# Kernel optimization log

Measured on AMD Instinct MI355X. Metric: run time of the kernel, lower is better.

Reference implementation:

```python
import jax, jax.numpy as jnp
import numpy as np

B, T, HORIZON = 64, 12, 12
N, E, K, H = 1024, 8, 3, 64
DIN, DOUT, YCOV = 1, 1, 1


def setup_inputs() -> dict:
    key = jax.random.key(0)
    ks = jax.random.split(key, 8)

    def xavier(k, shape):
        std = (2.0 / (shape[0] + shape[1])) ** 0.5
        return jax.random.normal(k, shape, jnp.float32) * std

    return {
        "x": jax.random.normal(ks[0], (B, T, N, DIN), jnp.float32),
        "y_cov": jax.random.normal(ks[1], (B, HORIZON, N, YCOV), jnp.float32),
        "node_embeddings": jax.random.normal(ks[2], (N, E), jnp.float32),
        "enc_gate_W": xavier(ks[3], (K * (DIN + H), 2 * H)),
        "enc_gate_b": jnp.zeros((2 * H,), jnp.float32),
        "enc_upd_W": xavier(ks[4], (K * (DIN + H), H)),
        "enc_upd_b": jnp.zeros((H,), jnp.float32),
        "dec_gate_W": xavier(ks[5], (K * (DOUT + YCOV + H), 2 * H)),
        "dec_gate_b": jnp.zeros((2 * H,), jnp.float32),
        "dec_upd_W": xavier(ks[6], (K * (DOUT + YCOV + H), H)),
        "dec_upd_b": jnp.zeros((H,), jnp.float32),
        "proj_W": xavier(ks[7], (H, DOUT)),
        "proj_b": jnp.zeros((DOUT,), jnp.float32),
    }


def _cheb(support, k):
    # Chebyshev polynomial set: T0=I, T1=A, Tk = 2*A@T_{k-1} - T_{k-2}
    mats = [jnp.eye(support.shape[0], dtype=support.dtype), support]
    for _ in range(2, k):
        mats.append(2.0 * (support @ mats[-1]) - mats[-2])
    return jnp.stack(mats)  # [K, N, N]


def _gcn(x, supports, W, b):
    # x: [B,N,C]; supports: [K,N,N] -> gather [B,N,K,C], concat k-major as in torch.cat
    xg = jnp.einsum('knm,bmc->bnkc', supports, x)
    Bb, Nn, Kk, Cc = xg.shape
    return xg.reshape(Bb, Nn, Kk * Cc) @ W + b


def _cell(x, state, supports, gW, gb, uW, ub):
    zr = jax.nn.sigmoid(_gcn(jnp.concatenate([x, state], axis=-1), supports, gW, gb))
    z, r = jnp.split(zr, 2, axis=-1)
    hc = jnp.tanh(_gcn(jnp.concatenate([x, z * state], axis=-1), supports, uW, ub))
    return r * state + (1.0 - r) * hc


def reference(x, y_cov, node_embeddings, enc_gate_W, enc_gate_b, enc_upd_W,
              enc_upd_b, dec_gate_W, dec_gate_b, dec_upd_W, dec_upd_b,
              proj_W, proj_b):
    # adaptive adjacency: softmax(relu(E E^T), axis=1)
    support = jax.nn.softmax(jax.nn.relu(node_embeddings @ node_embeddings.T), axis=1)
    supports = _cheb(support, K)

    # encoder over T_in steps (single rnn layer)
    h0 = jnp.zeros((x.shape[0], N, H), x.dtype)

    def enc_step(h, xt):
        h = _cell(xt, h, supports, enc_gate_W, enc_gate_b, enc_upd_W, enc_upd_b)
        return h, None

    h_t, _ = jax.lax.scan(enc_step, h0, jnp.swapaxes(x, 0, 1))

    go0 = jnp.zeros((x.shape[0], N, DOUT), x.dtype)

    def dec_step(carry, yt):
        go, h = carry
        h = _cell(jnp.concatenate([go, yt], axis=-1), h, supports,
                  dec_gate_W, dec_gate_b, dec_upd_W, dec_upd_b)
        go = h @ proj_W + proj_b
        return (go, h), go

    _, outs = jax.lax.scan(dec_step, (go0, h_t), jnp.swapaxes(y_cov, 0, 1))
    return jnp.swapaxes(outs, 0, 1)  # [B, horizon, N, output_dim]
```

## Files before the change

kernel.cpp:

```cpp
#include <hip/hip_runtime.h>


typedef __attribute__((ext_vector_type(8))) short bf16x8;
typedef __attribute__((ext_vector_type(4))) float f32x4;
typedef __attribute__((ext_vector_type(4))) unsigned short u16x4;

__device__ __forceinline__ float b2f(unsigned short u) {
    union { unsigned int i; float f; } v; v.i = ((unsigned int)u) << 16; return v.f;
}
__device__ __forceinline__ unsigned short f2b(float f) {
    union { float f; unsigned int i; } v; v.f = f;
    unsigned int r = v.i + 0x7FFFu + ((v.i >> 16) & 1u);
    return (unsigned short)(r >> 16);
}

#define GLOAD_LDS16(g, l) __builtin_amdgcn_global_load_lds( \
    (const __attribute__((address_space(1))) void*)(g),     \
    (__attribute__((address_space(3))) void*)(l), 16, 0, 0)

__global__ __launch_bounds__(256) void gemm_bt(
    const unsigned short* __restrict__ P, int lda,
    const unsigned short* __restrict__ QT, int ldb,
    unsigned short* __restrict__ C, int ldc,
    int K, float scale)
{
    __shared__ __align__(16) unsigned short As[128 * 32];
    __shared__ __align__(16) unsigned short Bs[128 * 32];
    const int tid = threadIdx.x;
    const int m0 = blockIdx.y << 7, n0 = blockIdx.x << 7;
    const int w = tid >> 6, l = tid & 63;
    const int wm = (w >> 1) << 6, wn = (w & 1) << 6;
    const int lr = l & 15, lq = l >> 4;
    const int arow = tid >> 2, ak = (tid & 3) << 3;
    f32x4 acc[4][4] = {};

    for (int k0 = 0; k0 < K; k0 += 32) {
#pragma unroll
        for (int p = 0; p < 2; ++p)
            GLOAD_LDS16(P + (size_t)(m0 + arow + (p << 6)) * lda + k0 + ak,
                        &As[((arow + (p << 6)) << 5) + ak]);
#pragma unroll
        for (int p = 0; p < 2; ++p)
            GLOAD_LDS16(QT + (size_t)(n0 + arow + (p << 6)) * ldb + k0 + ak,
                        &Bs[((arow + (p << 6)) << 5) + ak]);
        __syncthreads();
        bf16x8 a[4], b[4];
#pragma unroll
        for (int i = 0; i < 4; ++i)
            a[i] = *(const bf16x8*)&As[((wm + (i << 4) + lr) << 5) + (lq << 3)];
#pragma unroll
        for (int j = 0; j < 4; ++j)
            b[j] = *(const bf16x8*)&Bs[((wn + (j << 4) + lr) << 5) + (lq << 3)];
#pragma unroll
        for (int i = 0; i < 4; ++i)
#pragma unroll
            for (int j = 0; j < 4; ++j)
                acc[i][j] = __builtin_amdgcn_mfma_f32_16x16x32_bf16(a[i], b[j], acc[i][j], 0, 0, 0);
        __syncthreads();
    }
#pragma unroll
    for (int i = 0; i < 4; ++i)
#pragma unroll
        for (int j = 0; j < 4; ++j)
#pragma unroll
            for (int r = 0; r < 4; ++r) {
                const int m = m0 + wm + (i << 4) + (lq << 2) + r;
                const int n = n0 + wn + (j << 4) + lr;
                C[(size_t)m * ldc + n] = f2b(acc[i][j][r] * scale);
            }
}

__global__ __launch_bounds__(256) void cell_gate(
    const unsigned short* __restrict__ AA, const unsigned short* __restrict__ XhT,
    const unsigned short* __restrict__ Hb, const unsigned short* __restrict__ WT,
    const float* __restrict__ bias, const float* __restrict__ wx,
    const float* __restrict__ xin, int t,
    const unsigned short* __restrict__ XSgT, int xsrow,
    const unsigned short* __restrict__ Go, const float* __restrict__ H32,
    const float* __restrict__ prW, const float* __restrict__ prb,
    float* __restrict__ Sgo,
    unsigned short* __restrict__ Zb, unsigned short* __restrict__ ZhT,
    float* __restrict__ R, int dec, int goflag)
{
    __shared__ __align__(16) unsigned short As[256 * 32];
    __shared__ __align__(16) unsigned short Bs[128 * 32];
    __shared__ __align__(16) unsigned short Shs[256 * 72];
    __shared__ float SgoS[256];
    const int tid = threadIdx.x;
    const int b = blockIdx.x >> 3, n0 = (blockIdx.x & 7) << 7;
    const int w = tid >> 6, l = tid & 63;
    const int lr = l & 15, lq = l >> 4;
    const int arow = tid >> 2, ak = (tid & 3) << 3;

    {
        const int wm = w << 6;
        f32x4 acc[4][4] = {};
        for (int k0 = 0; k0 < 1024; k0 += 32) {
#pragma unroll
            for (int p = 0; p < 4; ++p) {
                const int row = arow + (p << 6);
                const int grow = (p < 2) ? (n0 + row) : (896 + n0 + row);
                GLOAD_LDS16(AA + (size_t)grow * 1024 + k0 + ak, &As[(row << 5) + ak]);
            }
            GLOAD_LDS16(XhT + (size_t)((b << 6) + arow) * 1024 + k0 + ak,
                        &Bs[(arow << 5) + ak]);
            __syncthreads();
            bf16x8 a[4], bb[4];
#pragma unroll
            for (int i = 0; i < 4; ++i)
                a[i] = *(const bf16x8*)&As[((wm + (i << 4) + lr) << 5) + (lq << 3)];
#pragma unroll
            for (int j = 0; j < 4; ++j)
                bb[j] = *(const bf16x8*)&Bs[(((j << 4) + lr) << 5) + (lq << 3)];
#pragma unroll
            for (int i = 0; i < 4; ++i)
#pragma unroll
                for (int j = 0; j < 4; ++j)
                    acc[i][j] = __builtin_amdgcn_mfma_f32_16x16x32_bf16(a[i], bb[j], acc[i][j], 0, 0, 0);
            __syncthreads();
        }
#pragma unroll
        for (int i = 0; i < 4; ++i)
#pragma unroll
            for (int j = 0; j < 4; ++j)
#pragma unroll
                for (int r = 0; r < 4; ++r) {
                    const int m = wm + (i << 4) + (lq << 2) + r;
                    const int c = (j << 4) + lr;
                    Shs[m * 72 + c] = f2b(acc[i][j][r]);
                }
        if (dec) {
            float pw[4];
#pragma unroll
            for (int j = 0; j < 4; ++j) pw[j] = prW[(j << 4) + lr];
            const float pb0 = prb[0];
#pragma unroll
            for (int i = 0; i < 4; ++i)
#pragma unroll
                for (int r = 0; r < 4; ++r) {
                    float v = acc[i][0][r] * pw[0] + acc[i][1][r] * pw[1]
                            + acc[i][2][r] * pw[2] + acc[i][3][r] * pw[3];
                    v += __shfl_down(v, 8, 16);
                    v += __shfl_down(v, 4, 16);
                    v += __shfl_down(v, 2, 16);
                    v += __shfl_down(v, 1, 16);
                    if (lr == 0) {
                        const int m = wm + (i << 4) + (lq << 2) + r;
                        const int grow = (m < 128) ? (n0 + m) : (896 + n0 + m);
                        const float val = goflag
                            ? (v + pb0 * ((m < 128) ? 1.f : 2.f)) : 0.f;
                        Sgo[(size_t)grow * 64 + b] = val;
                        SgoS[m] = val;
                    }
                }
        }
    }

    const int wm2 = (w >> 1) << 6, wn2 = (w & 1) << 6;
    f32x4 acc2[4][4] = {};
    for (int kk0 = 0; kk0 < 192; kk0 += 32) {
#pragma unroll
        for (int p = 0; p < 2; ++p)
            GLOAD_LDS16(WT + (size_t)(arow + (p << 6)) * 192 + kk0 + ak,
                        &Bs[((arow + (p << 6)) << 5) + ak]);
        if (kk0 < 64) {
#pragma unroll
            for (int p = 0; p < 2; ++p)
                GLOAD_LDS16(Hb + ((size_t)(b << 10) + n0 + arow + (p << 6)) * 64 + kk0 + ak,
                            &As[((arow + (p << 6)) << 5) + ak]);
        }
        __syncthreads();
        bf16x8 a[4], bb[4];
        if (kk0 < 64) {
#pragma unroll
            for (int i = 0; i < 4; ++i)
                a[i] = *(const bf16x8*)&As[((wm2 + (i << 4) + lr) << 5) + (lq << 3)];
        } else {
            const int rowb = (kk0 >= 128) ? 128 : 0;
            const int c0 = kk0 & 63;
#pragma unroll
            for (int i = 0; i < 4; ++i)
                a[i] = *(const bf16x8*)&Shs[(rowb + wm2 + (i << 4) + lr) * 72 + c0 + (lq << 3)];
        }
#pragma unroll
        for (int j = 0; j < 4; ++j)
            bb[j] = *(const bf16x8*)&Bs[((wn2 + (j << 4) + lr) << 5) + (lq << 3)];
#pragma unroll
        for (int i = 0; i < 4; ++i)
#pragma unroll
            for (int j = 0; j < 4; ++j)
                acc2[i][j] = __builtin_amdgcn_mfma_f32_16x16x32_bf16(a[i], bb[j], acc2[i][j], 0, 0, 0);
        __syncthreads();
    }

#pragma unroll
    for (int i = 0; i < 4; ++i) {
        const int nb_loc = wm2 + (i << 4) + (lq << 2);
        const int node_base = n0 + nb_loc;
        float c0[4], c1[4], c2[4], c3[4], c4[4], c5[4];
        for (int r = 0; r < 4; ++r) {
            const int node = node_base + r;
            if (!dec) {
                c0[r] = xin[((b * 12 + t) << 10) + node];
                c1[r] = b2f(XSgT[(size_t)(xsrow + t * 64 + b) * 2048 + node]);
                c2[r] = b2f(XSgT[(size_t)(xsrow + t * 64 + b) * 2048 + 1024 + node]);
                c3[r] = c4[r] = c5[r] = 0.f;
            } else {
                c0[r] = b2f(Go[(b << 10) + node]);
                c1[r] = xin[((b * 12 + t) << 10) + node];
                c2[r] = SgoS[nb_loc + r];
                c3[r] = b2f(XSgT[(size_t)(xsrow + t * 64 + b) * 2048 + node]);
                c4[r] = SgoS[128 + nb_loc + r];
                c5[r] = b2f(XSgT[(size_t)(xsrow + t * 64 + b) * 2048 + 1024 + node]);
            }
        }
#pragma unroll
        for (int j = 0; j < 4; ++j) {
            const int jc = wn2 + (j << 4) + lr;
            const float bj = bias[jc];
            const float w0 = wx[jc], w1 = wx[128 + jc], w2 = wx[256 + jc];
            float w3 = 0.f, w4 = 0.f, w5 = 0.f;
            if (dec) { w3 = wx[384 + jc]; w4 = wx[512 + jc]; w5 = wx[640 + jc]; }
            if (jc < 64) {
                u16x4 pack;
                for (int r = 0; r < 4; ++r) {
                    float v = acc2[i][j][r] + bj + c0[r] * w0 + c1[r] * w1 + c2[r] * w2
                              + c3[r] * w3 + c4[r] * w4 + c5[r] * w5;
                    float g = 1.f / (1.f + __expf(-v));
                    const int node = node_base + r;
                    const size_t idx = ((size_t)(b << 10) + node) * 64 + jc;
                    float zh = g * H32[idx];
                    unsigned short zb = f2b(zh);
                    Zb[idx] = zb;
                    pack[r] = zb;
                }
                *(u16x4*)&ZhT[(size_t)((b << 6) + jc) * 1024 + node_base] = pack;
            } else {
                for (int r = 0; r < 4; ++r) {
                    float v = acc2[i][j][r] + bj + c0[r] * w0 + c1[r] * w1 + c2[r] * w2
                              + c3[r] * w3 + c4[r] * w4 + c5[r] * w5;
                    float g = 1.f / (1.f + __expf(-v));
                    const int node = node_base + r;
                    R[((size_t)(b << 10) + node) * 64 + (jc - 64)] = g;
                }
            }
        }
    }
}

__global__ __launch_bounds__(256) void cell_update(
    const unsigned short* __restrict__ AA, const unsigned short* __restrict__ ZhT,
    const unsigned short* __restrict__ Zb, const unsigned short* __restrict__ WT,
    const float* __restrict__ bias, const float* __restrict__ wx,
    const float* __restrict__ xin, int t,
    const unsigned short* __restrict__ XSgT, int xsrow,
    const float* __restrict__ Sgo, const float* __restrict__ Rg,
    float* __restrict__ H32, unsigned short* __restrict__ Hb,
    unsigned short* __restrict__ XhT,
    const float* __restrict__ prW, const float* __restrict__ prb,
    unsigned short* __restrict__ Go, float* __restrict__ outp, int dec)
{
    __shared__ __align__(16) unsigned short As[256 * 32];
    __shared__ __align__(16) unsigned short Bs[64 * 32];
    __shared__ __align__(16) unsigned short Shs[256 * 72];
    const int tid = threadIdx.x;
    const int b = blockIdx.x >> 3, n0 = (blockIdx.x & 7) << 7;
    const int w = tid >> 6, l = tid & 63;
    const int lr = l & 15, lq = l >> 4;
    const int arow = tid >> 2, ak = (tid & 3) << 3;

    {
        const int wm = w << 6;
        f32x4 acc[4][4] = {};
        for (int k0 = 0; k0 < 1024; k0 += 32) {
#pragma unroll
            for (int p = 0; p < 4; ++p) {
                const int row = arow + (p << 6);
                const int grow = (p < 2) ? (n0 + row) : (896 + n0 + row);
                GLOAD_LDS16(AA + (size_t)grow * 1024 + k0 + ak, &As[(row << 5) + ak]);
            }
            GLOAD_LDS16(ZhT + (size_t)((b << 6) + arow) * 1024 + k0 + ak,
                        &Bs[(arow << 5) + ak]);
            __syncthreads();
            bf16x8 a[4], bb[4];
#pragma unroll
            for (int i = 0; i < 4; ++i)
                a[i] = *(const bf16x8*)&As[((wm + (i << 4) + lr) << 5) + (lq << 3)];
#pragma unroll
            for (int j = 0; j < 4; ++j)
                bb[j] = *(const bf16x8*)&Bs[(((j << 4) + lr) << 5) + (lq << 3)];
#pragma unroll
            for (int i = 0; i < 4; ++i)
#pragma unroll
                for (int j = 0; j < 4; ++j)
                    acc[i][j] = __builtin_amdgcn_mfma_f32_16x16x32_bf16(a[i], bb[j], acc[i][j], 0, 0, 0);
            __syncthreads();
        }
#pragma unroll
        for (int i = 0; i < 4; ++i)
#pragma unroll
            for (int j = 0; j < 4; ++j)
#pragma unroll
                for (int r = 0; r < 4; ++r) {
                    const int m = wm + (i << 4) + (lq << 2) + r;
                    const int c = (j << 4) + lr;
                    Shs[m * 72 + c] = f2b(acc[i][j][r]);
                }
    }

    const int wm2 = w << 5;
    f32x4 acc2[2][4] = {};
    for (int kk0 = 0; kk0 < 192; kk0 += 32) {
        GLOAD_LDS16(WT + (size_t)arow * 192 + kk0 + ak, &Bs[(arow << 5) + ak]);
        if (kk0 < 64) {
#pragma unroll
            for (int p = 0; p < 2; ++p)
                GLOAD_LDS16(Zb + ((size_t)(b << 10) + n0 + arow + (p << 6)) * 64 + kk0 + ak,
                            &As[((arow + (p << 6)) << 5) + ak]);
        }
        __syncthreads();
        bf16x8 a[2], bb[4];
        if (kk0 < 64) {
#pragma unroll
            for (int i = 0; i < 2; ++i)
                a[i] = *(const bf16x8*)&As[((wm2 + (i << 4) + lr) << 5) + (lq << 3)];
        } else {
            const int rowb = (kk0 >= 128) ? 128 : 0;
            const int c0 = kk0 & 63;
#pragma unroll
            for (int i = 0; i < 2; ++i)
                a[i] = *(const bf16x8*)&Shs[(rowb + wm2 + (i << 4) + lr) * 72 + c0 + (lq << 3)];
        }
#pragma unroll
        for (int j = 0; j < 4; ++j)
            bb[j] = *(const bf16x8*)&Bs[(((j << 4) + lr) << 5) + (lq << 3)];
#pragma unroll
        for (int i = 0; i < 2; ++i)
#pragma unroll
            for (int j = 0; j < 4; ++j)
                acc2[i][j] = __builtin_amdgcn_mfma_f32_16x16x32_bf16(a[i], bb[j], acc2[i][j], 0, 0, 0);
        __syncthreads();
    }

    float pw[4];
    if (dec) {
#pragma unroll
        for (int j = 0; j < 4; ++j) pw[j] = prW[(j << 4) + lr];
    }

#pragma unroll
    for (int i = 0; i < 2; ++i) {
        const int node_base = n0 + wm2 + (i << 4) + (lq << 2);
        float c0[4], c1[4], c2[4], c3[4], c4[4], c5[4];
        for (int r = 0; r < 4; ++r) {
            const int node = node_base + r;
            if (!dec) {
                c0[r] = xin[((b * 12 + t) << 10) + node];
                c1[r] = b2f(XSgT[(size_t)(xsrow + t * 64 + b) * 2048 + node]);
                c2[r] = b2f(XSgT[(size_t)(xsrow + t * 64 + b) * 2048 + 1024 + node]);
                c3[r] = c4[r] = c5[r] = 0.f;
            } else {
                c0[r] = b2f(Go[(b << 10) + node]);
                c1[r] = xin[((b * 12 + t) << 10) + node];
                c2[r] = Sgo[(size_t)node * 64 + b];
                c3[r] = b2f(XSgT[(size_t)(xsrow + t * 64 + b) * 2048 + node]);
                c4[r] = Sgo[(size_t)(1024 + node) * 64 + b];
                c5[r] = b2f(XSgT[(size_t)(xsrow + t * 64 + b) * 2048 + 1024 + node]);
            }
        }
        float psum[4] = {0.f, 0.f, 0.f, 0.f};
#pragma unroll
        for (int j = 0; j < 4; ++j) {
            const int jc = (j << 4) + lr;
            const float bj = bias[jc];
            const float w0 = wx[jc], w1 = wx[64 + jc], w2 = wx[128 + jc];
            float w3 = 0.f, w4 = 0.f, w5 = 0.f;
            if (dec) { w3 = wx[192 + jc]; w4 = wx[256 + jc]; w5 = wx[320 + jc]; }
            u16x4 pack;
            for (int r = 0; r < 4; ++r) {
                float v = acc2[i][j][r] + bj + c0[r] * w0 + c1[r] * w1 + c2[r] * w2
                          + c3[r] * w3 + c4[r] * w4 + c5[r] * w5;
                float hc = tanhf(v);
                const int node = node_base + r;
                const size_t idx = ((size_t)(b << 10) + node) * 64 + jc;
                float rr = Rg[idx];
                float hn = rr * H32[idx] + (1.f - rr) * hc;
                H32[idx] = hn;
                unsigned short hb = f2b(hn);
                Hb[idx] = hb;
                pack[r] = hb;
                if (dec) psum[r] += hn * pw[j];
            }
            *(u16x4*)&XhT[(size_t)((b << 6) + jc) * 1024 + node_base] = pack;
        }
        if (dec) {
#pragma unroll
            for (int r = 0; r < 4; ++r) {
                float v = psum[r];
                v += __shfl_down(v, 8, 16);
                v += __shfl_down(v, 4, 16);
                v += __shfl_down(v, 2, 16);
                v += __shfl_down(v, 1, 16);
                if (lr == 0) {
                    const int node = node_base + r;
                    const float go = v + prb[0];
                    Go[(b << 10) + node] = f2b(go);
                    outp[((size_t)(b * 12 + t) << 10) + node] = go;
                }
            }
        }
    }
}

__global__ __launch_bounds__(256) void adj_softmax(
    const float* __restrict__ E, unsigned short* __restrict__ A)
{
    __shared__ float Es[8192];
    __shared__ float vals[1024];
    __shared__ float red[8];
    const int tid = threadIdx.x;
    const int r = blockIdx.x;
    for (int i = tid; i < 8192; i += 256) Es[i] = E[i];
    __syncthreads();
    float er[8];
#pragma unroll
    for (int e = 0; e < 8; ++e) er[e] = Es[(r << 3) + e];
    float lmax = -1e30f;
    for (int c = tid; c < 1024; c += 256) {
        float s = 0.f;
#pragma unroll
        for (int e = 0; e < 8; ++e) s += er[e] * Es[(c << 3) + e];
        s = fmaxf(s, 0.f);
        vals[c] = s;
        lmax = fmaxf(lmax, s);
    }
    for (int off = 32; off; off >>= 1) lmax = fmaxf(lmax, __shfl_down(lmax, off, 64));
    if ((tid & 63) == 0) red[tid >> 6] = lmax;
    __syncthreads();
    const float m = fmaxf(fmaxf(red[0], red[1]), fmaxf(red[2], red[3]));
    float lsum = 0.f;
    for (int c = tid; c < 1024; c += 256) {
        float e = __expf(vals[c] - m);
        vals[c] = e;
        lsum += e;
    }
    for (int off = 32; off; off >>= 1) lsum += __shfl_down(lsum, off, 64);
    if ((tid & 63) == 0) red[4 + (tid >> 6)] = lsum;
    __syncthreads();
    const float inv = 1.f / (red[4] + red[5] + red[6] + red[7]);
    for (int c = tid; c < 1024; c += 256)
        A[(r << 10) + c] = f2b(vals[c] * inv);
}

__global__ __launch_bounds__(256) void transpose_bf16(
    const unsigned short* __restrict__ src, unsigned short* __restrict__ dst)
{
    __shared__ unsigned short tile[64][65];
    const int bx = blockIdx.x & 15, by = blockIdx.x >> 4;
    const int x0 = bx << 6, y0 = by << 6;
    for (int i = threadIdx.x; i < 4096; i += 256) {
        const int r = i >> 6, c = i & 63;
        tile[r][c] = src[((y0 + r) << 10) + x0 + c];
    }
    __syncthreads();
    for (int i = threadIdx.x; i < 4096; i += 256) {
        const int r = i >> 6, c = i & 63;
        dst[((x0 + r) << 10) + y0 + c] = tile[c][r];
    }
}

__global__ __launch_bounds__(256) void build_xall(
    const float* __restrict__ x, const float* __restrict__ y,
    unsigned short* __restrict__ XallT)
{
    const int id = blockIdx.x * 256 + threadIdx.x;
    const int row = id >> 10, n = id & 1023;
    int t, b;
    const float* src;
    if (row < 768) { t = row >> 6; b = row & 63; src = x; }
    else { const int rr = row - 768; t = rr >> 6; b = rr & 63; src = y; }
    XallT[id] = f2b(src[((b * 12 + t) << 10) + n]);
}

__global__ __launch_bounds__(256) void wprep(
    const float* egW, const float* egb,
    const float* euW, const float* eub,
    const float* dgW, const float* dgb,
    const float* duW, const float* dub,
    const float* pW, const float* pb,
    unsigned short* WgTe, unsigned short* WuTe, unsigned short* WgTd, unsigned short* WuTd,
    float* wxge, float* wxue, float* wxgd, float* wxud,
    float* bge, float* bue, float* bgd, float* bud,
    float* projW, float* projb)
{
    const int tid0 = blockIdx.x * 256 + threadIdx.x;
    const int stride = 256 * gridDim.x;
    for (int i = tid0; i < 128 * 192; i += stride) {
        const int j = i / 192, kk = i % 192, k = kk >> 6, c = kk & 63;
        float v = egW[(k * 65 + 1 + c) * 128 + j];
        if (k == 0) v -= egW[(131 + c) * 128 + j];
        WgTe[i] = f2b(v);
    }
    for (int i = tid0; i < 64 * 192; i += stride) {
        const int j = i / 192, kk = i % 192, k = kk >> 6, c = kk & 63;
        float v = euW[(k * 65 + 1 + c) * 64 + j];
        if (k == 0) v -= euW[(131 + c) * 64 + j];
        WuTe[i] = f2b(v);
    }
    for (int i = tid0; i < 128 * 192; i += stride) {
        const int j = i / 192, kk = i % 192, k = kk >> 6, c = kk & 63;
        float v = dgW[(k * 66 + 2 + c) * 128 + j];
        if (k == 0) v -= dgW[(134 + c) * 128 + j];
        WgTd[i] = f2b(v);
    }
    for (int i = tid0; i < 64 * 192; i += stride) {
        const int j = i / 192, kk = i % 192, k = kk >> 6, c = kk & 63;
        float v = duW[(k * 66 + 2 + c) * 64 + j];
        if (k == 0) v -= duW[(134 + c) * 64 + j];
        WuTd[i] = f2b(v);
    }
    for (int i = tid0; i < 384; i += stride) {
        const int k = i >> 7, j = i & 127;
        float v;
        if (k == 0) v = egW[j] - egW[130 * 128 + j];
        else if (k == 1) v = egW[65 * 128 + j];
        else v = egW[130 * 128 + j];
        wxge[i] = v;
    }
    for (int i = tid0; i < 192; i += stride) {
        const int k = i >> 6, j = i & 63;
        float v;
        if (k == 0) v = euW[j] - euW[130 * 64 + j];
        else if (k == 1) v = euW[65 * 64 + j];
        else v = euW[130 * 64 + j];
        wxue[i] = v;
    }
    for (int i = tid0; i < 768; i += stride) {
        const int k = i >> 7, j = i & 127;
        float v;
        switch (k) {
            case 0: v = dgW[j] - dgW[132 * 128 + j]; break;
            case 1: v = dgW[128 + j] - dgW[133 * 128 + j]; break;
            case 2: v = dgW[66 * 128 + j]; break;
            case 3: v = dgW[67 * 128 + j]; break;
            case 4: v = dgW[132 * 128 + j]; break;
            default: v = dgW[133 * 128 + j]; break;
        }
        wxgd[i] = v;
    }
    for (int i = tid0; i < 384; i += stride) {
        const int k = i >> 6, j = i & 63;
        float v;
        switch (k) {
            case 0: v = duW[j] - duW[132 * 64 + j]; break;
            case 1: v = duW[64 + j] - duW[133 * 64 + j]; break;
            case 2: v = duW[66 * 64 + j]; break;
            case 3: v = duW[67 * 64 + j]; break;
            case 4: v = duW[132 * 64 + j]; break;
            default: v = duW[133 * 64 + j]; break;
        }
        wxud[i] = v;
    }
    for (int i = tid0; i < 128; i += stride) bge[i] = egb[i];
    for (int i = tid0; i < 64; i += stride) bue[i] = eub[i];
    for (int i = tid0; i < 128; i += stride) bgd[i] = dgb[i];
    for (int i = tid0; i < 64; i += stride) bud[i] = dub[i];
    for (int i = tid0; i < 64; i += stride) projW[i] = pW[i];
    if (tid0 == 0) projb[0] = pb[0];
}

extern "C" void kernel_launch(void* const* d_in, const int* in_sizes, int n_in,
                              void* d_out, int out_size, void* d_ws, size_t ws_size,
                              hipStream_t stream)
{
    (void)in_sizes; (void)n_in; (void)out_size; (void)ws_size;
    const float* x    = (const float*)d_in[0];
    const float* ycov = (const float*)d_in[1];
    const float* E    = (const float*)d_in[2];
    const float* egW  = (const float*)d_in[3];
    const float* egb  = (const float*)d_in[4];
    const float* euW  = (const float*)d_in[5];
    const float* eub  = (const float*)d_in[6];
    const float* dgW  = (const float*)d_in[7];
    const float* dgb  = (const float*)d_in[8];
    const float* duW  = (const float*)d_in[9];
    const float* dub  = (const float*)d_in[10];
    const float* pW   = (const float*)d_in[11];
    const float* pb   = (const float*)d_in[12];
    float* out = (float*)d_out;

    size_t off = 0;
    auto carve = [&](size_t bytes) -> void* {
        void* p = (char*)d_ws + off;
        off += (bytes + 255) & ~(size_t)255;
        return p;
    };
    unsigned short* AA    = (unsigned short*)carve(2048ull * 1024 * 2);
    unsigned short* XSgT  = (unsigned short*)carve(1536ull * 2048 * 2);
    unsigned short* XhT   = (unsigned short*)carve(4096ull * 1024 * 2);
    unsigned short* ZhT   = (unsigned short*)carve(4096ull * 1024 * 2);
    unsigned short* Hb    = (unsigned short*)carve(65536ull * 64 * 2);
    float*          H32   = (float*)carve(65536ull * 64 * 4);
    unsigned short* Zb    = (unsigned short*)carve(65536ull * 64 * 2);
    float*          R     = (float*)carve(65536ull * 64 * 4);
    float*          Sgo   = (float*)carve(2048ull * 64 * 4);
    unsigned short* Go    = (unsigned short*)carve(65536ull * 2);
    unsigned short* WgTe  = (unsigned short*)carve(128ull * 192 * 2);
    unsigned short* WuTe  = (unsigned short*)carve(64ull * 192 * 2);
    unsigned short* WgTd  = (unsigned short*)carve(128ull * 192 * 2);
    unsigned short* WuTd  = (unsigned short*)carve(64ull * 192 * 2);
    float* wxge = (float*)carve(384 * 4);
    float* wxue = (float*)carve(192 * 4);
    float* wxgd = (float*)carve(768 * 4);
    float* wxud = (float*)carve(384 * 4);
    float* bge  = (float*)carve(128 * 4);
    float* bue  = (float*)carve(64 * 4);
    float* bgd  = (float*)carve(128 * 4);
    float* bud  = (float*)carve(64 * 4);
    float* prW  = (float*)carve(64 * 4);
    float* prb  = (float*)carve(4);
    unsigned short* AT    = Zb;
    unsigned short* XallT = Zb + 1024ull * 1024;

    hipMemsetAsync(XhT, 0, 4096ull * 1024 * 2, stream);
    hipMemsetAsync(Hb, 0, 65536ull * 64 * 2, stream);
    hipMemsetAsync(H32, 0, 65536ull * 64 * 4, stream);
    hipMemsetAsync(Go, 0, 65536ull * 2, stream);

    adj_softmax<<<1024, 256, 0, stream>>>(E, AA);
    transpose_bf16<<<256, 256, 0, stream>>>(AA, AT);
    gemm_bt<<<dim3(8, 8), 256, 0, stream>>>(AA, 1024, AT, 1024, AA + 1024 * 1024, 1024, 1024, 2.0f);
    build_xall<<<6144, 256, 0, stream>>>(x, ycov, XallT);
    gemm_bt<<<dim3(16, 12), 256, 0, stream>>>(XallT, 1024, AA, 1024, XSgT, 2048, 1024, 1.0f);
    wprep<<<64, 256, 0, stream>>>(egW, egb, euW, eub, dgW, dgb, duW, dub, pW, pb,
                                  WgTe, WuTe, WgTd, WuTd, wxge, wxue, wxgd, wxud,
                                  bge, bue, bgd, bud, prW, prb);

    for (int t = 0; t < 12; ++t) {
        cell_gate<<<512, 256, 0, stream>>>(AA, XhT, Hb, WgTe, bge, wxge, x, t, XSgT, 0,
                                           Go, H32, prW, prb, Sgo, Zb, ZhT, R, 0, 0);
        cell_update<<<512, 256, 0, stream>>>(AA, ZhT, Zb, WuTe, bue, wxue, x, t, XSgT, 0,
                                             Sgo, R, H32, Hb, XhT, prW, prb, Go, out, 0);
    }
    for (int t = 0; t < 12; ++t) {
        cell_gate<<<512, 256, 0, stream>>>(AA, XhT, Hb, WgTd, bgd, wxgd, ycov, t, XSgT, 768,
                                           Go, H32, prW, prb, Sgo, Zb, ZhT, R, 1, t > 0 ? 1 : 0);
        cell_update<<<512, 256, 0, stream>>>(AA, ZhT, Zb, WuTd, bud, wxud, ycov, t, XSgT, 768,
                                             Sgo, R, H32, Hb, XhT, prW, prb, Go, out, 1);
    }
}
```

Before: 2.455 ms.

## Load MFMA operands directly from global memory instead of staging through LDS

Both cell kernels now read the A/B MFMA fragments straight from global memory (AA, XhT/ZhT, Hb/Zb, weights), replacing the global_load_lds staging into shared tiles and the two barriers per k-step. This removes LDS staging traffic and synchronisation and frees LDS for occupancy, relying on L1/L2 to serve the redundant reads across waves. The gate kernel also reads the hidden state from the bf16 copy instead of the fp32 H32 array, which cuts bandwidth but lowers the precision of z*h. The cost is uncoalesced 16-byte strided global loads with no explicit reuse, so latency may be exposed.

```diff
diff --git a/kernel.cpp b/kernel.cpp
--- a/kernel.cpp
+++ b/kernel.cpp
@@ -76,48 +76,36 @@
     const float* __restrict__ bias, const float* __restrict__ wx,
     const float* __restrict__ xin, int t,
     const unsigned short* __restrict__ XSgT, int xsrow,
-    const unsigned short* __restrict__ Go, const float* __restrict__ H32,
+    const unsigned short* __restrict__ Go,
     const float* __restrict__ prW, const float* __restrict__ prb,
     float* __restrict__ Sgo,
     unsigned short* __restrict__ Zb, unsigned short* __restrict__ ZhT,
     float* __restrict__ R, int dec, int goflag)
 {
-    __shared__ __align__(16) unsigned short As[256 * 32];
-    __shared__ __align__(16) unsigned short Bs[128 * 32];
     __shared__ __align__(16) unsigned short Shs[256 * 72];
     __shared__ float SgoS[256];
     const int tid = threadIdx.x;
     const int b = blockIdx.x >> 3, n0 = (blockIdx.x & 7) << 7;
     const int w = tid >> 6, l = tid & 63;
     const int lr = l & 15, lq = l >> 4;
-    const int arow = tid >> 2, ak = (tid & 3) << 3;
 
     {
-        const int wm = w << 6;
+        const int wmP = w << 6;
+        const int rowoff = (w >= 2) ? (896 + n0) : n0;
         f32x4 acc[4][4] = {};
         for (int k0 = 0; k0 < 1024; k0 += 32) {
-#pragma unroll
-            for (int p = 0; p < 4; ++p) {
-                const int row = arow + (p << 6);
-                const int grow = (p < 2) ? (n0 + row) : (896 + n0 + row);
-                GLOAD_LDS16(AA + (size_t)grow * 1024 + k0 + ak, &As[(row << 5) + ak]);
-            }
-            GLOAD_LDS16(XhT + (size_t)((b << 6) + arow) * 1024 + k0 + ak,
-                        &Bs[(arow << 5) + ak]);
-            __syncthreads();
             bf16x8 a[4], bb[4];
 #pragma unroll
             for (int i = 0; i < 4; ++i)
-                a[i] = *(const bf16x8*)&As[((wm + (i << 4) + lr) << 5) + (lq << 3)];
+                a[i] = *(const bf16x8*)(AA + (size_t)(rowoff + wmP + (i << 4) + lr) * 1024 + k0 + (lq << 3));
 #pragma unroll
             for (int j = 0; j < 4; ++j)
-                bb[j] = *(const bf16x8*)&Bs[(((j << 4) + lr) << 5) + (lq << 3)];
+                bb[j] = *(const bf16x8*)(XhT + (size_t)((b << 6) + (j << 4) + lr) * 1024 + k0 + (lq << 3));
 #pragma unroll
             for (int i = 0; i < 4; ++i)
 #pragma unroll
                 for (int j = 0; j < 4; ++j)
                     acc[i][j] = __builtin_amdgcn_mfma_f32_16x16x32_bf16(a[i], bb[j], acc[i][j], 0, 0, 0);
-            __syncthreads();
         }
 #pragma unroll
         for (int i = 0; i < 4; ++i)
@@ -125,7 +113,7 @@
             for (int j = 0; j < 4; ++j)
 #pragma unroll
                 for (int r = 0; r < 4; ++r) {
-                    const int m = wm + (i << 4) + (lq << 2) + r;
+                    const int m = wmP + (i << 4) + (lq << 2) + r;
                     const int c = (j << 4) + lr;
                     Shs[m * 72 + c] = f2b(acc[i][j][r]);
                 }
@@ -145,7 +133,7 @@
                     v += __shfl_down(v, 2, 16);
                     v += __shfl_down(v, 1, 16);
                     if (lr == 0) {
-                        const int m = wm + (i << 4) + (lq << 2) + r;
+                        const int m = wmP + (i << 4) + (lq << 2) + r;
                         const int grow = (m < 128) ? (n0 + m) : (896 + n0 + m);
                         const float val = goflag
                             ? (v + pb0 * ((m < 128) ? 1.f : 2.f)) : 0.f;
@@ -155,26 +143,16 @@
                 }
         }
     }
+    __syncthreads();
 
     const int wm2 = (w >> 1) << 6, wn2 = (w & 1) << 6;
     f32x4 acc2[4][4] = {};
     for (int kk0 = 0; kk0 < 192; kk0 += 32) {
-#pragma unroll
-        for (int p = 0; p < 2; ++p)
-            GLOAD_LDS16(WT + (size_t)(arow + (p << 6)) * 192 + kk0 + ak,
-                        &Bs[((arow + (p << 6)) << 5) + ak]);
-        if (kk0 < 64) {
-#pragma unroll
-            for (int p = 0; p < 2; ++p)
-                GLOAD_LDS16(Hb + ((size_t)(b << 10) + n0 + arow + (p << 6)) * 64 + kk0 + ak,
-                            &As[((arow + (p << 6)) << 5) + ak]);
-        }
-        __syncthreads();
         bf16x8 a[4], bb[4];
         if (kk0 < 64) {
 #pragma unroll
             for (int i = 0; i < 4; ++i)
-                a[i] = *(const bf16x8*)&As[((wm2 + (i << 4) + lr) << 5) + (lq << 3)];
+                a[i] = *(const bf16x8*)(Hb + ((size_t)(b << 10) + n0 + wm2 + (i << 4) + lr) * 64 + kk0 + (lq << 3));
         } else {
             const int rowb = (kk0 >= 128) ? 128 : 0;
             const int c0 = kk0 & 63;
@@ -184,13 +162,12 @@
         }
 #pragma unroll
         for (int j = 0; j < 4; ++j)
-            bb[j] = *(const bf16x8*)&Bs[((wn2 + (j << 4) + lr) << 5) + (lq << 3)];
+            bb[j] = *(const bf16x8*)(WT + (size_t)(wn2 + (j << 4) + lr) * 192 + kk0 + (lq << 3));
 #pragma unroll
         for (int i = 0; i < 4; ++i)
 #pragma unroll
             for (int j = 0; j < 4; ++j)
                 acc2[i][j] = __builtin_amdgcn_mfma_f32_16x16x32_bf16(a[i], bb[j], acc2[i][j], 0, 0, 0);
-        __syncthreads();
     }
 
 #pragma unroll
@@ -229,7 +206,7 @@
                     float g = 1.f / (1.f + __expf(-v));
                     const int node = node_base + r;
                     const size_t idx = ((size_t)(b << 10) + node) * 64 + jc;
-                    float zh = g * H32[idx];
+                    float zh = g * b2f(Hb[idx]);
                     unsigned short zb = f2b(zh);
                     Zb[idx] = zb;
                     pack[r] = zb;
@@ -260,41 +237,29 @@
     const float* __restrict__ prW, const float* __restrict__ prb,
     unsigned short* __restrict__ Go, float* __restrict__ outp, int dec)
 {
-    __shared__ __align__(16) unsigned short As[256 * 32];
-    __shared__ __align__(16) unsigned short Bs[64 * 32];
     __shared__ __align__(16) unsigned short Shs[256 * 72];
     const int tid = threadIdx.x;
     const int b = blockIdx.x >> 3, n0 = (blockIdx.x & 7) << 7;
     const int w = tid >> 6, l = tid & 63;
     const int lr = l & 15, lq = l >> 4;
-    const int arow = tid >> 2, ak = (tid & 3) << 3;
 
     {
-        const int wm = w << 6;
+        const int wmP = w << 6;
+        const int rowoff = (w >= 2) ? (896 + n0) : n0;
         f32x4 acc[4][4] = {};
         for (int k0 = 0; k0 < 1024; k0 += 32) {
-#pragma unroll
-            for (int p = 0; p < 4; ++p) {
-                const int row = arow + (p << 6);
-                const int grow = (p < 2) ? (n0 + row) : (896 + n0 + row);
-                GLOAD_LDS16(AA + (size_t)grow * 1024 + k0 + ak, &As[(row << 5) + ak]);
-            }
-            GLOAD_LDS16(ZhT + (size_t)((b << 6) + arow) * 1024 + k0 + ak,
-                        &Bs[(arow << 5) + ak]);
-            __syncthreads();
             bf16x8 a[4], bb[4];
 #pragma unroll
             for (int i = 0; i < 4; ++i)
-                a[i] = *(const bf16x8*)&As[((wm + (i << 4) + lr) << 5) + (lq << 3)];
+                a[i] = *(const bf16x8*)(AA + (size_t)(rowoff + wmP + (i << 4) + lr) * 1024 + k0 + (lq << 3));
 #pragma unroll
             for (int j = 0; j < 4; ++j)
-                bb[j] = *(const bf16x8*)&Bs[(((j << 4) + lr) << 5) + (lq << 3)];
+                bb[j] = *(const bf16x8*)(ZhT + (size_t)((b << 6) + (j << 4) + lr) * 1024 + k0 + (lq << 3));
 #pragma unroll
             for (int i = 0; i < 4; ++i)
 #pragma unroll
                 for (int j = 0; j < 4; ++j)
                     acc[i][j] = __builtin_amdgcn_mfma_f32_16x16x32_bf16(a[i], bb[j], acc[i][j], 0, 0, 0);
-            __syncthreads();
         }
 #pragma unroll
         for (int i = 0; i < 4; ++i)
@@ -302,28 +267,21 @@
             for (int j = 0; j < 4; ++j)
 #pragma unroll
                 for (int r = 0; r < 4; ++r) {
-                    const int m = wm + (i << 4) + (lq << 2) + r;
+                    const int m = wmP + (i << 4) + (lq << 2) + r;
                     const int c = (j << 4) + lr;
                     Shs[m * 72 + c] = f2b(acc[i][j][r]);
                 }
     }
+    __syncthreads();
 
     const int wm2 = w << 5;
     f32x4 acc2[2][4] = {};
     for (int kk0 = 0; kk0 < 192; kk0 += 32) {
-        GLOAD_LDS16(WT + (size_t)arow * 192 + kk0 + ak, &Bs[(arow << 5) + ak]);
-        if (kk0 < 64) {
-#pragma unroll
-            for (int p = 0; p < 2; ++p)
-                GLOAD_LDS16(Zb + ((size_t)(b << 10) + n0 + arow + (p << 6)) * 64 + kk0 + ak,
-                            &As[((arow + (p << 6)) << 5) + ak]);
-        }
-        __syncthreads();
         bf16x8 a[2], bb[4];
         if (kk0 < 64) {
 #pragma unroll
             for (int i = 0; i < 2; ++i)
-                a[i] = *(const bf16x8*)&As[((wm2 + (i << 4) + lr) << 5) + (lq << 3)];
+                a[i] = *(const bf16x8*)(Zb + ((size_t)(b << 10) + n0 + wm2 + (i << 4) + lr) * 64 + kk0 + (lq << 3));
         } else {
             const int rowb = (kk0 >= 128) ? 128 : 0;
             const int c0 = kk0 & 63;
@@ -333,13 +291,12 @@
         }
 #pragma unroll
         for (int j = 0; j < 4; ++j)
-            bb[j] = *(const bf16x8*)&Bs[(((j << 4) + lr) << 5) + (lq << 3)];
+            bb[j] = *(const bf16x8*)(WT + (size_t)((j << 4) + lr) * 192 + kk0 + (lq << 3));
 #pragma unroll
         for (int i = 0; i < 2; ++i)
 #pragma unroll
             for (int j = 0; j < 4; ++j)
                 acc2[i][j] = __builtin_amdgcn_mfma_f32_16x16x32_bf16(a[i], bb[j], acc2[i][j], 0, 0, 0);
-        __syncthreads();
     }
 
     float pw[4];
@@ -638,13 +595,13 @@
 
     for (int t = 0; t < 12; ++t) {
         cell_gate<<<512, 256, 0, stream>>>(AA, XhT, Hb, WgTe, bge, wxge, x, t, XSgT, 0,
-                                           Go, H32, prW, prb, Sgo, Zb, ZhT, R, 0, 0);
+                                           Go, prW, prb, Sgo, Zb, ZhT, R, 0, 0);
         cell_update<<<512, 256, 0, stream>>>(AA, ZhT, Zb, WuTe, bue, wxue, x, t, XSgT, 0,
                                              Sgo, R, H32, Hb, XhT, prW, prb, Go, out, 0);
     }
     for (int t = 0; t < 12; ++t) {
         cell_gate<<<512, 256, 0, stream>>>(AA, XhT, Hb, WgTd, bgd, wxgd, ycov, t, XSgT, 768,
-                                           Go, H32, prW, prb, Sgo, Zb, ZhT, R, 1, t > 0 ? 1 : 0);
+                                           Go, prW, prb, Sgo, Zb, ZhT, R, 1, t > 0 ? 1 : 0);
         cell_update<<<512, 256, 0, stream>>>(AA, ZhT, Zb, WuTd, bud, wxud, ycov, t, XSgT, 768,
                                              Sgo, R, H32, Hb, XhT, prW, prb, Go, out, 1);
     }
```

Result: slower. 4.080 ms (+66.2%).

## Drop fp32 hidden state, store gate R in bf16, alias LDS buffers

Applied to the files above, without the earlier changes.

Removes the fp32 hidden-state copy H32 and reads the bf16 Hb instead. The reset gate R is now stored as bf16, which cuts global traffic per step. Shared memory is unioned so that As, Shs and SgoS share one buffer, and launch bounds request 4 blocks per CU to raise occupancy. The second small GEMM now loads operands directly from global memory instead of staging them through LDS, which removes its barriers. The cost is lower precision in the recurrent state, which accumulates over 24 steps, and possibly uncoalesced direct global loads.

```diff
diff --git a/kernel.cpp b/kernel.cpp
--- a/kernel.cpp
+++ b/kernel.cpp
@@ -70,22 +70,23 @@
             }
 }
 
-__global__ __launch_bounds__(256) void cell_gate(
+__global__ __launch_bounds__(256, 4) void cell_gate(
     const unsigned short* __restrict__ AA, const unsigned short* __restrict__ XhT,
     const unsigned short* __restrict__ Hb, const unsigned short* __restrict__ WT,
     const float* __restrict__ bias, const float* __restrict__ wx,
     const float* __restrict__ xin, int t,
     const unsigned short* __restrict__ XSgT, int xsrow,
-    const unsigned short* __restrict__ Go, const float* __restrict__ H32,
+    const unsigned short* __restrict__ Go,
     const float* __restrict__ prW, const float* __restrict__ prb,
     float* __restrict__ Sgo,
     unsigned short* __restrict__ Zb, unsigned short* __restrict__ ZhT,
-    float* __restrict__ R, int dec, int goflag)
-{
-    __shared__ __align__(16) unsigned short As[256 * 32];
-    __shared__ __align__(16) unsigned short Bs[128 * 32];
-    __shared__ __align__(16) unsigned short Shs[256 * 72];
-    __shared__ float SgoS[256];
+    unsigned short* __restrict__ R, int dec, int goflag)
+{
+    __shared__ __align__(16) unsigned char smem[37888];
+    unsigned short* As  = (unsigned short*)smem;
+    unsigned short* Bs  = (unsigned short*)(smem + 16384);
+    unsigned short* Shs = (unsigned short*)smem;
+    float* SgoS = (float*)(smem + 36864);
     const int tid = threadIdx.x;
     const int b = blockIdx.x >> 3, n0 = (blockIdx.x & 7) << 7;
     const int w = tid >> 6, l = tid & 63;
@@ -155,26 +156,16 @@
                 }
         }
     }
+    __syncthreads();
 
     const int wm2 = (w >> 1) << 6, wn2 = (w & 1) << 6;
     f32x4 acc2[4][4] = {};
     for (int kk0 = 0; kk0 < 192; kk0 += 32) {
-#pragma unroll
-        for (int p = 0; p < 2; ++p)
-            GLOAD_LDS16(WT + (size_t)(arow + (p << 6)) * 192 + kk0 + ak,
-                        &Bs[((arow + (p << 6)) << 5) + ak]);
-        if (kk0 < 64) {
-#pragma unroll
-            for (int p = 0; p < 2; ++p)
-                GLOAD_LDS16(Hb + ((size_t)(b << 10) + n0 + arow + (p << 6)) * 64 + kk0 + ak,
-                            &As[((arow + (p << 6)) << 5) + ak]);
-        }
-        __syncthreads();
         bf16x8 a[4], bb[4];
         if (kk0 < 64) {
 #pragma unroll
             for (int i = 0; i < 4; ++i)
-                a[i] = *(const bf16x8*)&As[((wm2 + (i << 4) + lr) << 5) + (lq << 3)];
+                a[i] = *(const bf16x8*)(Hb + ((size_t)(b << 10) + n0 + wm2 + (i << 4) + lr) * 64 + kk0 + (lq << 3));
         } else {
             const int rowb = (kk0 >= 128) ? 128 : 0;
             const int c0 = kk0 & 63;
@@ -184,13 +175,12 @@
         }
 #pragma unroll
         for (int j = 0; j < 4; ++j)
-            bb[j] = *(const bf16x8*)&Bs[((wn2 + (j << 4) + lr) << 5) + (lq << 3)];
+            bb[j] = *(const bf16x8*)(WT + (size_t)(wn2 + (j << 4) + lr) * 192 + kk0 + (lq << 3));
 #pragma unroll
         for (int i = 0; i < 4; ++i)
 #pragma unroll
             for (int j = 0; j < 4; ++j)
                 acc2[i][j] = __builtin_amdgcn_mfma_f32_16x16x32_bf16(a[i], bb[j], acc2[i][j], 0, 0, 0);
-        __syncthreads();
     }
 
 #pragma unroll
@@ -229,7 +219,7 @@
                     float g = 1.f / (1.f + __expf(-v));
                     const int node = node_base + r;
                     const size_t idx = ((size_t)(b << 10) + node) * 64 + jc;
-                    float zh = g * H32[idx];
+                    float zh = g * b2f(Hb[idx]);
                     unsigned short zb = f2b(zh);
                     Zb[idx] = zb;
                     pack[r] = zb;
@@ -241,28 +231,28 @@
                               + c3[r] * w3 + c4[r] * w4 + c5[r] * w5;
                     float g = 1.f / (1.f + __expf(-v));
                     const int node = node_base + r;
-                    R[((size_t)(b << 10) + node) * 64 + (jc - 64)] = g;
+                    R[((size_t)(b << 10) + node) * 64 + (jc - 64)] = f2b(g);
                 }
             }
         }
     }
 }
 
-__global__ __launch_bounds__(256) void cell_update(
+__global__ __launch_bounds__(256, 4) void cell_update(
     const unsigned short* __restrict__ AA, const unsigned short* __restrict__ ZhT,
     const unsigned short* __restrict__ Zb, const unsigned short* __restrict__ WT,
     const float* __restrict__ bias, const float* __restrict__ wx,
     const float* __restrict__ xin, int t,
     const unsigned short* __restrict__ XSgT, int xsrow,
-    const float* __restrict__ Sgo, const float* __restrict__ Rg,
-    float* __restrict__ H32, unsigned short* __restrict__ Hb,
-    unsigned short* __restrict__ XhT,
+    const float* __restrict__ Sgo, const unsigned short* __restrict__ Rg,
+    unsigned short* __restrict__ Hb, unsigned short* __restrict__ XhT,
     const float* __restrict__ prW, const float* __restrict__ prb,
     unsigned short* __restrict__ Go, float* __restrict__ outp, int dec)
 {
-    __shared__ __align__(16) unsigned short As[256 * 32];
-    __shared__ __align__(16) unsigned short Bs[64 * 32];
-    __shared__ __align__(16) unsigned short Shs[256 * 72];
+    __shared__ __align__(16) unsigned char smem[36864];
+    unsigned short* As  = (unsigned short*)smem;
+    unsigned short* Bs  = (unsigned short*)(smem + 16384);
+    unsigned short* Shs = (unsigned short*)smem;
     const int tid = threadIdx.x;
     const int b = blockIdx.x >> 3, n0 = (blockIdx.x & 7) << 7;
     const int w = tid >> 6, l = tid & 63;
@@ -307,23 +297,16 @@
                     Shs[m * 72 + c] = f2b(acc[i][j][r]);
                 }
     }
+    __syncthreads();
 
     const int wm2 = w << 5;
     f32x4 acc2[2][4] = {};
     for (int kk0 = 0; kk0 < 192; kk0 += 32) {
-        GLOAD_LDS16(WT + (size_t)arow * 192 + kk0 + ak, &Bs[(arow << 5) + ak]);
-        if (kk0 < 64) {
-#pragma unroll
-            for (int p = 0; p < 2; ++p)
-                GLOAD_LDS16(Zb + ((size_t)(b << 10) + n0 + arow + (p << 6)) * 64 + kk0 + ak,
-                            &As[((arow + (p << 6)) << 5) + ak]);
-        }
-        __syncthreads();
         bf16x8 a[2], bb[4];
         if (kk0 < 64) {
 #pragma unroll
             for (int i = 0; i < 2; ++i)
-                a[i] = *(const bf16x8*)&As[((wm2 + (i << 4) + lr) << 5) + (lq << 3)];
+                a[i] = *(const bf16x8*)(Zb + ((size_t)(b << 10) + n0 + wm2 + (i << 4) + lr) * 64 + kk0 + (lq << 3));
         } else {
             const int rowb = (kk0 >= 128) ? 128 : 0;
             const int c0 = kk0 & 63;
@@ -333,13 +316,12 @@
         }
 #pragma unroll
         for (int j = 0; j < 4; ++j)
-            bb[j] = *(const bf16x8*)&Bs[(((j << 4) + lr) << 5) + (lq << 3)];
+            bb[j] = *(const bf16x8*)(WT + (size_t)((j << 4) + lr) * 192 + kk0 + (lq << 3));
 #pragma unroll
         for (int i = 0; i < 2; ++i)
 #pragma unroll
             for (int j = 0; j < 4; ++j)
                 acc2[i][j] = __builtin_amdgcn_mfma_f32_16x16x32_bf16(a[i], bb[j], acc2[i][j], 0, 0, 0);
-        __syncthreads();
     }
 
     float pw[4];
@@ -383,9 +365,8 @@
                 float hc = tanhf(v);
                 const int node = node_base + r;
                 const size_t idx = ((size_t)(b << 10) + node) * 64 + jc;
-                float rr = Rg[idx];
-                float hn = rr * H32[idx] + (1.f - rr) * hc;
-                H32[idx] = hn;
+                float rr = b2f(Rg[idx]);
+                float hn = rr * b2f(Hb[idx]) + (1.f - rr) * hc;
                 unsigned short hb = f2b(hn);
                 Hb[idx] = hb;
                 pack[r] = hb;
@@ -600,9 +581,8 @@
     unsigned short* XhT   = (unsigned short*)carve(4096ull * 1024 * 2);
     unsigned short* ZhT   = (unsigned short*)carve(4096ull * 1024 * 2);
     unsigned short* Hb    = (unsigned short*)carve(65536ull * 64 * 2);
-    float*          H32   = (float*)carve(65536ull * 64 * 4);
     unsigned short* Zb    = (unsigned short*)carve(65536ull * 64 * 2);
-    float*          R     = (float*)carve(65536ull * 64 * 4);
+    unsigned short* R     = (unsigned short*)carve(65536ull * 64 * 2);
     float*          Sgo   = (float*)carve(2048ull * 64 * 4);
     unsigned short* Go    = (unsigned short*)carve(65536ull * 2);
     unsigned short* WgTe  = (unsigned short*)carve(128ull * 192 * 2);
@@ -624,7 +604,6 @@
 
     hipMemsetAsync(XhT, 0, 4096ull * 1024 * 2, stream);
     hipMemsetAsync(Hb, 0, 65536ull * 64 * 2, stream);
-    hipMemsetAsync(H32, 0, 65536ull * 64 * 4, stream);
     hipMemsetAsync(Go, 0, 65536ull * 2, stream);
 
     adj_softmax<<<1024, 256, 0, stream>>>(E, AA);
@@ -638,14 +617,14 @@
 
     for (int t = 0; t < 12; ++t) {
         cell_gate<<<512, 256, 0, stream>>>(AA, XhT, Hb, WgTe, bge, wxge, x, t, XSgT, 0,
-                                           Go, H32, prW, prb, Sgo, Zb, ZhT, R, 0, 0);
+                                           Go, prW, prb, Sgo, Zb, ZhT, R, 0, 0);
         cell_update<<<512, 256, 0, stream>>>(AA, ZhT, Zb, WuTe, bue, wxue, x, t, XSgT, 0,
-                                             Sgo, R, H32, Hb, XhT, prW, prb, Go, out, 0);
+                                             Sgo, R, Hb, XhT, prW, prb, Go, out, 0);
     }
     for (int t = 0; t < 12; ++t) {
         cell_gate<<<512, 256, 0, stream>>>(AA, XhT, Hb, WgTd, bgd, wxgd, ycov, t, XSgT, 768,
-                                           Go, H32, prW, prb, Sgo, Zb, ZhT, R, 1, t > 0 ? 1 : 0);
+                                           Go, prW, prb, Sgo, Zb, ZhT, R, 1, t > 0 ? 1 : 0);
         cell_update<<<512, 256, 0, stream>>>(AA, ZhT, Zb, WuTd, bud, wxud, ycov, t, XSgT, 768,
-                                             Sgo, R, H32, Hb, XhT, prW, prb, Go, out, 1);
-    }
-}
+                                             Sgo, R, Hb, XhT, prW, prb, Go, out, 1);
+    }
+}
```

New measurement: 2.529 ms. 1.03x slower.
